# Optimization experiments

Hardware: AMD Instinct MI355X
Metric: run time of the kernel (lower is better)

The kernel has to match this reference:

```python
import jax, jax.numpy as jnp
import numpy as np

NUM_JOINTS = 33
EPS = 1e-5
# MediaPipe 33-landmark pose skeleton connections
SKELETON_EDGES = np.array([
    [0,1],[1,2],[2,3],[3,7],[0,4],[4,5],[5,6],[6,8],[9,10],
    [11,12],[11,13],[13,15],[15,17],[15,19],[15,21],[17,19],
    [12,14],[14,16],[16,18],[16,20],[16,22],[18,20],
    [11,23],[12,24],[23,24],[23,25],[24,26],[25,27],[26,28],
    [27,29],[28,30],[29,31],[30,32],[27,31],[28,32]], dtype=np.int64)


def _batched_edges(B):
    und = np.concatenate([SKELETON_EDGES, SKELETON_EDGES[:, ::-1]], axis=0)
    loops = np.stack([np.arange(NUM_JOINTS)] * 2, axis=1)
    e = np.concatenate([und, loops], axis=0)  # [103, 2] per graph (incl. self loops)
    eb = (e[None, :, :] + (np.arange(B) * NUM_JOINTS)[:, None, None]).reshape(-1, 2)
    return jnp.asarray(eb[:, 0], dtype=jnp.int32), jnp.asarray(eb[:, 1], dtype=jnp.int32)


def setup_inputs() -> dict:
    key = jax.random.key(0)
    B, N, F, H, L = 4096, NUM_JOINTS, 256, 256, 4
    ks = jax.random.split(key, 20)
    d = {"x": jax.random.normal(ks[0], (B, N, F), dtype=jnp.float32)}
    dims = [(F, H), (H, H), (H, H)]
    i = 1
    for li, (di, do) in enumerate(dims):
        d[f"w{li}"] = jax.random.normal(ks[i], (di, do), dtype=jnp.float32) * 0.05; i += 1
        d[f"b{li}"] = jnp.zeros((do,), dtype=jnp.float32)
        d[f"g{li}"] = jnp.ones((do,), dtype=jnp.float32)
        d[f"be{li}"] = jnp.zeros((do,), dtype=jnp.float32)
    d["wh"] = jax.random.normal(ks[i], (H, H), dtype=jnp.float32) * 0.05; i += 1
    d["bh"] = jnp.zeros((H,), dtype=jnp.float32)
    d["wc"] = jax.random.normal(ks[i], (H, L), dtype=jnp.float32) * 0.05; i += 1
    d["bc"] = jnp.zeros((L,), dtype=jnp.float32)
    src, dst = _batched_edges(B)
    d["src"], d["dst"] = src, dst
    return d


def _gcn_conv(x, W, b, src, dst, norm, num_nodes):
    h = x @ W                          # [NN, out]
    msg = h[src] * norm[:, None]       # gather + scale
    agg = jax.ops.segment_sum(msg, dst, num_segments=num_nodes)
    return agg + b


def _bn_relu(x, g, be):
    mu = jnp.mean(x, axis=0)
    var = jnp.mean((x - mu) ** 2, axis=0)  # biased, torch training BN
    return jax.nn.relu((x - mu) * jax.lax.rsqrt(var + EPS) * g + be)


def reference(x, w0, b0, g0, be0, w1, b1, g1, be1, w2, b2, g2, be2, wh, bh, wc, bc, src, dst):
    B, N, F = x.shape
    NN = B * N
    h = jnp.nan_to_num(x.reshape(NN, F))
    # symmetric GCN normalization D^{-1/2}(A+I)D^{-1/2}; self loops already in edge list
    deg = jax.ops.segment_sum(jnp.ones_like(src, dtype=h.dtype), dst, num_segments=NN)
    dinv = jax.lax.rsqrt(deg)
    norm = dinv[src] * dinv[dst]
    for W, b, g, be in ((w0, b0, g0, be0), (w1, b1, g1, be1), (w2, b2, g2, be2)):
        h = _gcn_conv(h, W, b, src, dst, norm, NN)
        h = _bn_relu(h, g, be)  # dropout: eval mode -> identity
    h = _gcn_conv(h, wh, bh, src, dst, norm, NN)
    pooled = h.reshape(B, N, -1).mean(axis=1)  # global mean pool per graph
    return pooled @ wc + bc
```

## Files before the change

### kernel.cpp

```cpp
#include <hip/hip_runtime.h>

typedef unsigned short u16;
typedef __attribute__((ext_vector_type(8))) short short8;
typedef __attribute__((ext_vector_type(4))) float floatx4;

#define NN_TOT 135168

static constexpr int NBCNT[33] = {2,2,2,2,2,2,2,1,1,1,1,3,3,2,2,4,4,2,2,2,2,1,1,3,3,2,2,3,3,2,2,2,2};
static constexpr int NBR[33][4] = {
 {1,4,0,0},{0,2,0,0},{1,3,0,0},{2,7,0,0},{0,5,0,0},{4,6,0,0},{5,8,0,0},
 {3,0,0,0},{6,0,0,0},{10,0,0,0},{9,0,0,0},
 {12,13,23,0},{11,14,24,0},{11,15,0,0},{12,16,0,0},
 {13,17,19,21},{14,18,20,22},
 {15,19,0,0},{16,20,0,0},{15,17,0,0},{16,18,0,0},{15,0,0,0},{16,0,0,0},
 {11,24,25,0},{12,23,26,0},{23,27,0,0},{24,28,0,0},
 {25,29,31,0},{26,30,32,0},{27,31,0,0},{28,32,0,0},{29,27,0,0},{30,28,0,0}};
static constexpr float R2 = 0.70710678f, R3 = 0.57735027f, R4 = 0.5f, R5 = 0.44721360f;
static constexpr float DINV[33] = {R3,R3,R3,R3,R3,R3,R3, R2,R2,R2,R2, R4,R4, R3,R3, R5,R5,
                                   R3,R3,R3,R3, R2,R2, R4,R4, R3,R3, R4,R4, R3,R3,R3,R3};

__device__ __forceinline__ float bf2f(u16 u) {
  unsigned int v = ((unsigned int)u) << 16; float f; __builtin_memcpy(&f, &v, 4); return f;
}
__device__ __forceinline__ u16 f2bf(float f) {
  unsigned int u; __builtin_memcpy(&u, &f, 4);
  return (u16)((u + 0x7fffu + ((u >> 16) & 1u)) >> 16);
}
__device__ __forceinline__ float ldin(const void* p, int i, int isbf) {
  return isbf ? bf2f(((const u16*)p)[i]) : ((const float*)p)[i];
}
__device__ __forceinline__ void gload_lds16(const u16* g, u16* l) {
  __builtin_amdgcn_global_load_lds((const __attribute__((address_space(1))) unsigned int*)g,
                                   (__attribute__((address_space(3))) unsigned int*)l, 16, 0, 0);
}

__global__ __launch_bounds__(256) void detect_kernel(const u16* __restrict__ x,
                                                     int* __restrict__ flag)
{
  __shared__ int cnt[256];
  const int t = threadIdx.x;
  int c = 0;
  for (int j = 0; j < 16; ++j) {
    u16 u = x[(t*16 + j)*2];
    int e = (u >> 7) & 0xFF;
    c += (e >= 118 && e <= 130) ? 1 : 0;
  }
  cnt[t] = c;
  __syncthreads();
  if (t == 0) {
    int s = 0;
    for (int i = 0; i < 256; ++i) s += cnt[i];
    *flag = (s > 2048) ? 1 : 0;
  }
}

__global__ __launch_bounds__(256) void transpose_kernel(const void* __restrict__ w0,
    const void* __restrict__ w1, const void* __restrict__ w2, u16* __restrict__ Wt,
    const int* __restrict__ flag)
{
  const int m = blockIdx.x >> 4;
  const int nb = (blockIdx.x & 15) * 16;
  const void* W = m == 0 ? w0 : (m == 1 ? w1 : w2);
  u16* O = Wt + (size_t)m * 65536;
  const int t = threadIdx.x;
  const int lane = t & 63, wv = t >> 6;
  const int isbf = *flag;
  if (isbf) {
    const u16* Wb = (const u16*)W;
#pragma unroll
    for (int nn = 0; nn < 4; ++nn) {
      const int n = nb + nn*4 + wv;
#pragma unroll
      for (int j = 0; j < 4; ++j) {
        const int k = lane + 64*j;
        O[n*256 + k] = Wb[k*256 + n];
      }
    }
  } else {
    const float* Wf = (const float*)W;
#pragma unroll
    for (int nn = 0; nn < 4; ++nn) {
      const int n = nb + nn*4 + wv;
#pragma unroll
      for (int j = 0; j < 4; ++j) {
        const int k = lane + 64*j;
        O[n*256 + k] = f2bf(Wf[k*256 + n]);
      }
    }
  }
}

__global__ __launch_bounds__(256) void init_kernel(const void* __restrict__ wh,
    const void* __restrict__ bh, const void* __restrict__ wc, const void* __restrict__ bc,
    float* __restrict__ wq, float* __restrict__ bq, float* __restrict__ repl,
    const int* __restrict__ flag)
{
  const int idx = blockIdx.x*256 + threadIdx.x;
  for (int i = idx; i < 3*64*512; i += 65*256) repl[i] = 0.f;
  const int isbf = *flag;
  const int t = threadIdx.x;
  const int lane = t & 63;
  if (blockIdx.x < 64) {
    const int r = blockIdx.x*4 + (t >> 6);
    float a0=0.f, a1=0.f, a2=0.f, a3=0.f;
#pragma unroll
    for (int j = 0; j < 4; ++j) {
      const int k = lane + 64*j;
      const float w = ldin(wh, r*256 + k, isbf);
      a0 += w*ldin(wc, k*4+0, isbf); a1 += w*ldin(wc, k*4+1, isbf);
      a2 += w*ldin(wc, k*4+2, isbf); a3 += w*ldin(wc, k*4+3, isbf);
    }
#pragma unroll
    for (int off = 32; off; off >>= 1) {
      a0 += __shfl_xor(a0, off); a1 += __shfl_xor(a1, off);
      a2 += __shfl_xor(a2, off); a3 += __shfl_xor(a3, off);
    }
    if (lane == 0) { wq[r*4+0]=a0; wq[r*4+1]=a1; wq[r*4+2]=a2; wq[r*4+3]=a3; }
  } else if (t < 64) {
    float s0=0.f, s1=0.f, s2=0.f, s3=0.f;
#pragma unroll
    for (int j = 0; j < 4; ++j) {
      const int k = lane + 64*j;
      const float b = ldin(bh, k, isbf);
      s0 += b*ldin(wc, k*4+0, isbf); s1 += b*ldin(wc, k*4+1, isbf);
      s2 += b*ldin(wc, k*4+2, isbf); s3 += b*ldin(wc, k*4+3, isbf);
    }
#pragma unroll
    for (int off = 32; off; off >>= 1) {
      s0 += __shfl_xor(s0, off); s1 += __shfl_xor(s1, off);
      s2 += __shfl_xor(s2, off); s3 += __shfl_xor(s3, off);
    }
    if (lane == 0) {
      bq[0] = s0 + ldin(bc, 0, isbf); bq[1] = s1 + ldin(bc, 1, isbf);
      bq[2] = s2 + ldin(bc, 2, isbf); bq[3] = s3 + ldin(bc, 3, isbf);
    }
  }
}

template<int ACT>
__global__ __launch_bounds__(256, 2) void gemm_kernel(
    const void* __restrict__ Ag, const u16* __restrict__ Bt,
    const float* __restrict__ fscale, const float* __restrict__ fshift,
    u16* __restrict__ T, const int* __restrict__ flag)
{
  __shared__ __align__(16) u16 sA[128*32];
  __shared__ __align__(16) u16 sB[256*32];
  const int tid = threadIdx.x;
  const int lane = tid & 63, wid = tid >> 6;
  const int wm = wid >> 1, wn = wid & 1;
  const size_t m0 = (size_t)blockIdx.x * 128;
  const int isbf = (ACT == 0) ? *flag : 1;

  floatx4 acc[4][8];
#pragma unroll
  for (int i = 0; i < 4; ++i)
#pragma unroll
    for (int j = 0; j < 8; ++j) acc[i][j] = (floatx4){0.f, 0.f, 0.f, 0.f};

  const int r0 = tid >> 2;
  const int c8 = (tid & 3) * 8;
  const int lr = lane >> 2;
  const int lc = (lane & 3) * 8;
  const int fr = lane & 15, q = lane >> 4;

  for (int kc = 0; kc < 8; ++kc) {
    const int k0 = kc * 32;
    __syncthreads();
    if (ACT == 0) {
      if (isbf) {
        const u16* Ab = (const u16*)Ag;
#pragma unroll
        for (int i = 0; i < 2; ++i)
          gload_lds16(Ab + (m0 + wid*32 + i*16 + lr)*256 + k0 + lc,
                      sA + (wid*32 + i*16)*32);
      } else {
        const float* Af = (const float*)Ag;
#pragma unroll
        for (int rr = 0; rr < 2; ++rr) {
          const int r = r0 + rr*64;
          float4 p0 = *(const float4*)(Af + (m0 + r)*256 + k0 + c8);
          float4 p1 = *(const float4*)(Af + (m0 + r)*256 + k0 + c8 + 4);
          u16 ov[8];
          ov[0]=f2bf(p0.x); ov[1]=f2bf(p0.y); ov[2]=f2bf(p0.z); ov[3]=f2bf(p0.w);
          ov[4]=f2bf(p1.x); ov[5]=f2bf(p1.y); ov[6]=f2bf(p1.z); ov[7]=f2bf(p1.w);
          *(uint4*)(sA + r*32 + c8) = *(const uint4*)ov;
        }
      }
    } else {
      const u16* Ab = (const u16*)Ag;
      float scv[8], shv[8];
#pragma unroll
      for (int j = 0; j < 8; ++j) { scv[j] = fscale[k0 + c8 + j]; shv[j] = fshift[k0 + c8 + j]; }
#pragma unroll
      for (int rr = 0; rr < 2; ++rr) {
        const int r = r0 + rr*64;
        uint4 pk = *(const uint4*)(Ab + (m0 + r)*256 + k0 + c8);
        const u16* us = (const u16*)&pk;
        u16 ov[8];
#pragma unroll
        for (int j = 0; j < 8; ++j) {
          float f = bf2f(us[j]);
          f = fmaxf(0.f, fmaf(f, scv[j], shv[j]));
          ov[j] = f2bf(f);
        }
        *(uint4*)(sA + r*32 + c8) = *(const uint4*)ov;
      }
    }
#pragma unroll
    for (int i = 0; i < 4; ++i)
      gload_lds16(Bt + (wid*64 + i*16 + lr)*256 + k0 + lc,
                  sB + (wid*64 + i*16)*32);
    __syncthreads();

    short8 a[4], b[8];
#pragma unroll
    for (int mf = 0; mf < 4; ++mf) a[mf] = *(const short8*)(sA + (wm*64 + mf*16 + fr)*32 + q*8);
#pragma unroll
    for (int nf = 0; nf < 8; ++nf) b[nf] = *(const short8*)(sB + (wn*128 + nf*16 + fr)*32 + q*8);
#pragma unroll
    for (int mf = 0; mf < 4; ++mf)
#pragma unroll
      for (int nf = 0; nf < 8; ++nf)
        acc[mf][nf] = __builtin_amdgcn_mfma_f32_16x16x32_bf16(a[mf], b[nf], acc[mf][nf], 0, 0, 0);
  }

#pragma unroll
  for (int mf = 0; mf < 4; ++mf)
#pragma unroll
    for (int nf = 0; nf < 8; ++nf)
#pragma unroll
      for (int r = 0; r < 4; ++r) {
        const size_t row = m0 + wm*64 + mf*16 + q*4 + r;
        const int col = wn*128 + nf*16 + fr;
        T[row*256 + col] = f2bf(acc[mf][nf][r]);
      }
}

__global__ __launch_bounds__(256) void agg_kernel(const u16* __restrict__ T,
    const void* __restrict__ bias, u16* __restrict__ H, float* __restrict__ repl,
    const int* __restrict__ flag)
{
  const int g = blockIdx.x, c = threadIdx.x;
  const int isbf = *flag;
  const u16* tg = T + (size_t)g * (33*256);
  u16* hg = H + (size_t)g * (33*256);
  float acc[33];
#pragma unroll
  for (int d = 0; d < 33; ++d) acc[d] = 0.f;
#pragma unroll
  for (int s = 0; s < 33; ++s) {
    float v = bf2f(tg[s*256 + c]) * DINV[s];
    acc[s] += v;
#pragma unroll
    for (int i = 0; i < NBCNT[s]; ++i) acc[NBR[s][i]] += v;
  }
  const float bv = ldin(bias, c, isbf);
  float s1 = 0.f, s2 = 0.f;
#pragma unroll
  for (int d = 0; d < 33; ++d) {
    float o = fmaf(acc[d], DINV[d], bv);
    hg[d*256 + c] = f2bf(o);
    s1 += o; s2 += o*o;
  }
  float* r1 = repl + (size_t)(g & 63) * 512;
  atomicAdd(r1 + c, s1);
  atomicAdd(r1 + 256 + c, s2);
}

__global__ __launch_bounds__(256) void statfin_kernel(const float* __restrict__ repl,
    const void* __restrict__ gamma, const void* __restrict__ beta, float* __restrict__ fs,
    const int* __restrict__ flag)
{
  const int c = threadIdx.x;
  const int isbf = *flag;
  float s1 = 0.f, s2 = 0.f;
  for (int r = 0; r < 64; ++r) { s1 += repl[r*512 + c]; s2 += repl[r*512 + 256 + c]; }
  const float inv = 1.f / (float)NN_TOT;
  const float mu = s1 * inv;
  const float var = s2 * inv - mu*mu;
  const float rs = rsqrtf(var + 1e-5f);
  const float sc = rs * ldin(gamma, c, isbf);
  fs[c] = sc;
  fs[256 + c] = ldin(beta, c, isbf) - mu * sc;
}

__global__ __launch_bounds__(256) void final_kernel(const u16* __restrict__ H,
    const float* __restrict__ fs, const float* __restrict__ wq,
    const float* __restrict__ bq, void* __restrict__ outp,
    const int* __restrict__ flag)
{
  const int g = blockIdx.x, c = threadIdx.x;
  const int isbf = *flag;
  const float sc = fs[c], sh = fs[256 + c];
  const u16* hg = H + (size_t)g * (33*256);
  float v = 0.f;
#pragma unroll
  for (int s = 0; s < 33; ++s) {
    float a = DINV[s];
#pragma unroll
    for (int i = 0; i < NBCNT[s]; ++i) a += DINV[NBR[s][i]];
    const float w = DINV[s] * a * (1.f/33.f);
    float x = bf2f(hg[s*256 + c]);
    x = fmaxf(0.f, fmaf(x, sc, sh));
    v += w * x;
  }
  float p0 = v*wq[c*4+0], p1 = v*wq[c*4+1], p2 = v*wq[c*4+2], p3 = v*wq[c*4+3];
#pragma unroll
  for (int off = 32; off; off >>= 1) {
    p0 += __shfl_xor(p0, off);
    p1 += __shfl_xor(p1, off);
    p2 += __shfl_xor(p2, off);
    p3 += __shfl_xor(p3, off);
  }
  __shared__ float sred[4][4];
  const int lane = c & 63, wid = c >> 6;
  if (lane == 0) { sred[wid][0]=p0; sred[wid][1]=p1; sred[wid][2]=p2; sred[wid][3]=p3; }
  __syncthreads();
  if (c < 4) {
    float r = sred[0][c] + sred[1][c] + sred[2][c] + sred[3][c] + bq[c];
    if (isbf) ((u16*)outp)[(size_t)g*4 + c] = f2bf(r);
    else      ((float*)outp)[(size_t)g*4 + c] = r;
  }
}

extern "C" void kernel_launch(void* const* d_in, const int* in_sizes, int n_in,
                              void* d_out, int out_size, void* d_ws, size_t ws_size,
                              hipStream_t stream)
{
  const void* x   = d_in[0];
  const void* w0  = d_in[1];
  const void* b0  = d_in[2];
  const void* g0  = d_in[3];
  const void* be0 = d_in[4];
  const void* w1  = d_in[5];
  const void* b1  = d_in[6];
  const void* g1  = d_in[7];
  const void* be1 = d_in[8];
  const void* w2  = d_in[9];
  const void* b2  = d_in[10];
  const void* g2  = d_in[11];
  const void* be2 = d_in[12];
  const void* wh  = d_in[13];
  const void* bh  = d_in[14];
  const void* wc  = d_in[15];
  const void* bc  = d_in[16];

  char* ws = (char*)d_ws;
  float* wq   = (float*)(ws + 0);
  float* bq   = (float*)(ws + 4096);
  float* fs   = (float*)(ws + 4608);
  int*   flag = (int*)  (ws + 12288);
  float* repl = (float*)(ws + 16384);
  u16*   Wt   = (u16*)  (ws + 409600);
  u16*   A    = (u16*)  (ws + 802816);
  (void)in_sizes; (void)n_in; (void)out_size; (void)ws_size;

  detect_kernel<<<1, 256, 0, stream>>>((const u16*)x, flag);
  transpose_kernel<<<48, 256, 0, stream>>>(w0, w1, w2, Wt, flag);
  init_kernel<<<65, 256, 0, stream>>>(wh, bh, wc, bc, wq, bq, repl, flag);

  gemm_kernel<0><<<1056, 256, 0, stream>>>(x, Wt, nullptr, nullptr, A, flag);
  agg_kernel<<<4096, 256, 0, stream>>>(A, b0, A, repl, flag);
  statfin_kernel<<<1, 256, 0, stream>>>(repl, g0, be0, fs, flag);
  gemm_kernel<1><<<1056, 256, 0, stream>>>(A, Wt + 65536, fs, fs + 256, A, flag);
  agg_kernel<<<4096, 256, 0, stream>>>(A, b1, A, repl + 32768, flag);
  statfin_kernel<<<1, 256, 0, stream>>>(repl + 32768, g1, be1, fs + 512, flag);
  gemm_kernel<1><<<1056, 256, 0, stream>>>(A, Wt + 131072, fs + 512, fs + 768, A, flag);
  agg_kernel<<<4096, 256, 0, stream>>>(A, b2, A, repl + 65536, flag);
  statfin_kernel<<<1, 256, 0, stream>>>(repl + 65536, g2, be2, fs + 1024, flag);
  final_kernel<<<4096, 256, 0, stream>>>(A, fs + 1024, wq, bq, d_out, flag);
}
```

Baseline: 454.2 us.

## Double-buffer GEMM LDS tiles and stage output through LDS for wide stores

Converts the GEMM main loop to a double-buffered scheme. The next K-chunk's global loads and the async LDS loads are issued before the MFMAs on the current buffer, and the BN/ReLU or fp32-to-bf16 conversion is written to the other buffer afterwards. This is meant to overlap memory latency with compute and cut one barrier per iteration. The epilogue now stages accumulator tiles through padded LDS so each thread writes 16-byte coalesced rows instead of scattered 2-byte stores. LDS use grows to 48KB per block, which may limit occupancy with launch_bounds(256,2). The scale and shift values are now reloaded per element inside finish rather than held in registers.

```diff
diff --git a/kernel.cpp b/kernel.cpp
--- a/kernel.cpp
+++ b/kernel.cpp
@@ -143,8 +143,9 @@
     const float* __restrict__ fscale, const float* __restrict__ fshift,
     u16* __restrict__ T, const int* __restrict__ flag)
 {
-  __shared__ __align__(16) u16 sA[128*32];
-  __shared__ __align__(16) u16 sB[256*32];
+  __shared__ __align__(16) u16 smem[24576];
+  u16* const sA0 = smem;
+  u16* const sB0 = smem + 8192;
   const int tid = threadIdx.x;
   const int lane = tid & 63, wid = tid >> 6;
   const int wm = wid >> 1, wn = wid & 1;
@@ -163,77 +164,108 @@
   const int lc = (lane & 3) * 8;
   const int fr = lane & 15, q = lane >> 4;
 
-  for (int kc = 0; kc < 8; ++kc) {
-    const int k0 = kc * 32;
-    __syncthreads();
-    if (ACT == 0) {
-      if (isbf) {
-        const u16* Ab = (const u16*)Ag;
-#pragma unroll
-        for (int i = 0; i < 2; ++i)
-          gload_lds16(Ab + (m0 + wid*32 + i*16 + lr)*256 + k0 + lc,
-                      sA + (wid*32 + i*16)*32);
-      } else {
-        const float* Af = (const float*)Ag;
-#pragma unroll
-        for (int rr = 0; rr < 2; ++rr) {
-          const int r = r0 + rr*64;
-          float4 p0 = *(const float4*)(Af + (m0 + r)*256 + k0 + c8);
-          float4 p1 = *(const float4*)(Af + (m0 + r)*256 + k0 + c8 + 4);
-          u16 ov[8];
-          ov[0]=f2bf(p0.x); ov[1]=f2bf(p0.y); ov[2]=f2bf(p0.z); ov[3]=f2bf(p0.w);
-          ov[4]=f2bf(p1.x); ov[5]=f2bf(p1.y); ov[6]=f2bf(p1.z); ov[7]=f2bf(p1.w);
-          *(uint4*)(sA + r*32 + c8) = *(const uint4*)ov;
-        }
+  const u16* Ab = (const u16*)Ag;
+  const float* Af = (const float*)Ag;
+
+  uint4  regA[2];
+  float4 regF[2][2];
+
+  auto issue = [&](int buf, int k0) {
+    if (ACT == 0 && isbf) {
+#pragma unroll
+      for (int i = 0; i < 2; ++i)
+        gload_lds16(Ab + (m0 + wid*32 + i*16 + lr)*256 + k0 + lc,
+                    sA0 + buf*4096 + (wid*32 + i*16)*32);
+    } else if (ACT == 0) {
+#pragma unroll
+      for (int rr = 0; rr < 2; ++rr) {
+        regF[rr][0] = *(const float4*)(Af + (m0 + r0 + rr*64)*256 + k0 + c8);
+        regF[rr][1] = *(const float4*)(Af + (m0 + r0 + rr*64)*256 + k0 + c8 + 4);
       }
     } else {
-      const u16* Ab = (const u16*)Ag;
-      float scv[8], shv[8];
-#pragma unroll
-      for (int j = 0; j < 8; ++j) { scv[j] = fscale[k0 + c8 + j]; shv[j] = fshift[k0 + c8 + j]; }
+#pragma unroll
+      for (int rr = 0; rr < 2; ++rr)
+        regA[rr] = *(const uint4*)(Ab + (m0 + r0 + rr*64)*256 + k0 + c8);
+    }
+#pragma unroll
+    for (int i = 0; i < 4; ++i)
+      gload_lds16(Bt + (wid*64 + i*16 + lr)*256 + k0 + lc,
+                  sB0 + buf*8192 + (wid*64 + i*16)*32);
+  };
+
+  auto finish = [&](int buf, int k0) {
+    if (ACT == 1) {
 #pragma unroll
       for (int rr = 0; rr < 2; ++rr) {
-        const int r = r0 + rr*64;
-        uint4 pk = *(const uint4*)(Ab + (m0 + r)*256 + k0 + c8);
-        const u16* us = (const u16*)&pk;
+        const u16* us = (const u16*)&regA[rr];
         u16 ov[8];
 #pragma unroll
         for (int j = 0; j < 8; ++j) {
           float f = bf2f(us[j]);
-          f = fmaxf(0.f, fmaf(f, scv[j], shv[j]));
+          f = fmaxf(0.f, fmaf(f, fscale[k0 + c8 + j], fshift[k0 + c8 + j]));
           ov[j] = f2bf(f);
         }
-        *(uint4*)(sA + r*32 + c8) = *(const uint4*)ov;
+        *(uint4*)(sA0 + buf*4096 + (r0 + rr*64)*32 + c8) = *(const uint4*)ov;
       }
-    }
-#pragma unroll
-    for (int i = 0; i < 4; ++i)
-      gload_lds16(Bt + (wid*64 + i*16 + lr)*256 + k0 + lc,
-                  sB + (wid*64 + i*16)*32);
-    __syncthreads();
+    } else if (ACT == 0 && !isbf) {
+#pragma unroll
+      for (int rr = 0; rr < 2; ++rr) {
+        u16 ov[8];
+        ov[0]=f2bf(regF[rr][0].x); ov[1]=f2bf(regF[rr][0].y);
+        ov[2]=f2bf(regF[rr][0].z); ov[3]=f2bf(regF[rr][0].w);
+        ov[4]=f2bf(regF[rr][1].x); ov[5]=f2bf(regF[rr][1].y);
+        ov[6]=f2bf(regF[rr][1].z); ov[7]=f2bf(regF[rr][1].w);
+        *(uint4*)(sA0 + buf*4096 + (r0 + rr*64)*32 + c8) = *(const uint4*)ov;
+      }
+    }
+  };
+
+  issue(0, 0);
+  finish(0, 0);
+  __syncthreads();
+
+  for (int kc = 0; kc < 8; ++kc) {
+    const int cur = kc & 1;
+    if (kc < 7) issue(cur ^ 1, (kc + 1) * 32);
 
     short8 a[4], b[8];
 #pragma unroll
-    for (int mf = 0; mf < 4; ++mf) a[mf] = *(const short8*)(sA + (wm*64 + mf*16 + fr)*32 + q*8);
-#pragma unroll
-    for (int nf = 0; nf < 8; ++nf) b[nf] = *(const short8*)(sB + (wn*128 + nf*16 + fr)*32 + q*8);
+    for (int mf = 0; mf < 4; ++mf)
+      a[mf] = *(const short8*)(sA0 + cur*4096 + (wm*64 + mf*16 + fr)*32 + q*8);
+#pragma unroll
+    for (int nf = 0; nf < 8; ++nf)
+      b[nf] = *(const short8*)(sB0 + cur*8192 + (wn*128 + nf*16 + fr)*32 + q*8);
 #pragma unroll
     for (int mf = 0; mf < 4; ++mf)
 #pragma unroll
       for (int nf = 0; nf < 8; ++nf)
         acc[mf][nf] = __builtin_amdgcn_mfma_f32_16x16x32_bf16(a[mf], b[nf], acc[mf][nf], 0, 0, 0);
-  }
-
-#pragma unroll
-  for (int mf = 0; mf < 4; ++mf)
+
+    if (kc < 7) { finish(cur ^ 1, (kc + 1) * 32); __syncthreads(); }
+  }
+
+  u16* const Ct = smem;
+  const int lrow = tid >> 3;
+  const int cg = (tid & 7) * 32;
+#pragma unroll
+  for (int mf = 0; mf < 4; ++mf) {
+    __syncthreads();
 #pragma unroll
     for (int nf = 0; nf < 8; ++nf)
 #pragma unroll
-      for (int r = 0; r < 4; ++r) {
-        const size_t row = m0 + wm*64 + mf*16 + q*4 + r;
-        const int col = wn*128 + nf*16 + fr;
-        T[row*256 + col] = f2bf(acc[mf][nf][r]);
-      }
+      for (int r = 0; r < 4; ++r)
+        Ct[(wm*16 + q*4 + r)*264 + wn*128 + nf*16 + fr] = f2bf(acc[mf][nf][r]);
+    __syncthreads();
+    const size_t grow = m0 + (size_t)((lrow >> 4) * 64 + mf*16 + (lrow & 15));
+    uint4 w0 = *(const uint4*)(Ct + lrow*264 + cg);
+    uint4 w1 = *(const uint4*)(Ct + lrow*264 + cg + 8);
+    uint4 w2 = *(const uint4*)(Ct + lrow*264 + cg + 16);
+    uint4 w3 = *(const uint4*)(Ct + lrow*264 + cg + 24);
+    *(uint4*)(T + grow*256 + cg)      = w0;
+    *(uint4*)(T + grow*256 + cg + 8)  = w1;
+    *(uint4*)(T + grow*256 + cg + 16) = w2;
+    *(uint4*)(T + grow*256 + cg + 24) = w3;
+  }
 }
 
 __global__ __launch_bounds__(256) void agg_kernel(const u16* __restrict__ T,
```

Result: slower. 479.2 us (+5.5%).

## Drop LDS staging in GEMM and load MFMA fragments directly from global

Applied to the files above, without the earlier changes.

The GEMM kernel no longer stages A and B tiles through shared memory. Each wave now owns 32 full rows across all 256 output columns, and it loads A and B fragments straight from global memory into registers, which removes both __syncthreads barriers. The aim is to cut LDS traffic and barrier stalls. The cost is that every wave re-reads the whole B matrix from global or cache through uncoalesced 16-byte loads, with less reuse between waves.

```diff
diff --git a/kernel.cpp b/kernel.cpp
--- a/kernel.cpp
+++ b/kernel.cpp
@@ -29,10 +29,6 @@
 __device__ __forceinline__ float ldin(const void* p, int i, int isbf) {
   return isbf ? bf2f(((const u16*)p)[i]) : ((const float*)p)[i];
 }
-__device__ __forceinline__ void gload_lds16(const u16* g, u16* l) {
-  __builtin_amdgcn_global_load_lds((const __attribute__((address_space(1))) unsigned int*)g,
-                                   (__attribute__((address_space(3))) unsigned int*)l, 16, 0, 0);
-}
 
 __global__ __launch_bounds__(256) void detect_kernel(const u16* __restrict__ x,
                                                      int* __restrict__ flag)
@@ -143,58 +139,53 @@
     const float* __restrict__ fscale, const float* __restrict__ fshift,
     u16* __restrict__ T, const int* __restrict__ flag)
 {
-  __shared__ __align__(16) u16 sA[128*32];
-  __shared__ __align__(16) u16 sB[256*32];
   const int tid = threadIdx.x;
-  const int lane = tid & 63, wid = tid >> 6;
-  const int wm = wid >> 1, wn = wid & 1;
+  const int lane = tid & 63, w = tid >> 6;
+  const int fr = lane & 15, q = lane >> 4;
   const size_t m0 = (size_t)blockIdx.x * 128;
+  const int rbase = w * 32;
   const int isbf = (ACT == 0) ? *flag : 1;
 
-  floatx4 acc[4][8];
-#pragma unroll
-  for (int i = 0; i < 4; ++i)
-#pragma unroll
-    for (int j = 0; j < 8; ++j) acc[i][j] = (floatx4){0.f, 0.f, 0.f, 0.f};
-
-  const int r0 = tid >> 2;
-  const int c8 = (tid & 3) * 8;
-  const int lr = lane >> 2;
-  const int lc = (lane & 3) * 8;
-  const int fr = lane & 15, q = lane >> 4;
+  const u16* Ab = (const u16*)Ag;
+  const float* Af = (const float*)Ag;
+
+  floatx4 acc[2][16];
+#pragma unroll
+  for (int i = 0; i < 2; ++i)
+#pragma unroll
+    for (int j = 0; j < 16; ++j) acc[i][j] = (floatx4){0.f, 0.f, 0.f, 0.f};
 
   for (int kc = 0; kc < 8; ++kc) {
     const int k0 = kc * 32;
-    __syncthreads();
+
+    short8 a[2];
     if (ACT == 0) {
       if (isbf) {
-        const u16* Ab = (const u16*)Ag;
-#pragma unroll
-        for (int i = 0; i < 2; ++i)
-          gload_lds16(Ab + (m0 + wid*32 + i*16 + lr)*256 + k0 + lc,
-                      sA + (wid*32 + i*16)*32);
+#pragma unroll
+        for (int mg = 0; mg < 2; ++mg)
+          a[mg] = *(const short8*)(Ab + (m0 + rbase + mg*16 + fr)*256 + k0 + q*8);
       } else {
-        const float* Af = (const float*)Ag;
-#pragma unroll
-        for (int rr = 0; rr < 2; ++rr) {
-          const int r = r0 + rr*64;
-          float4 p0 = *(const float4*)(Af + (m0 + r)*256 + k0 + c8);
-          float4 p1 = *(const float4*)(Af + (m0 + r)*256 + k0 + c8 + 4);
+#pragma unroll
+        for (int mg = 0; mg < 2; ++mg) {
+          const float* ap = Af + (m0 + rbase + mg*16 + fr)*256 + k0 + q*8;
+          float4 p0 = *(const float4*)(ap);
+          float4 p1 = *(const float4*)(ap + 4);
           u16 ov[8];
           ov[0]=f2bf(p0.x); ov[1]=f2bf(p0.y); ov[2]=f2bf(p0.z); ov[3]=f2bf(p0.w);
           ov[4]=f2bf(p1.x); ov[5]=f2bf(p1.y); ov[6]=f2bf(p1.z); ov[7]=f2bf(p1.w);
-          *(uint4*)(sA + r*32 + c8) = *(const uint4*)ov;
+          a[mg] = *(const short8*)ov;
         }
       }
     } else {
-      const u16* Ab = (const u16*)Ag;
-      float scv[8], shv[8];
-#pragma unroll
-      for (int j = 0; j < 8; ++j) { scv[j] = fscale[k0 + c8 + j]; shv[j] = fshift[k0 + c8 + j]; }
-#pragma unroll
-      for (int rr = 0; rr < 2; ++rr) {
-        const int r = r0 + rr*64;
-        uint4 pk = *(const uint4*)(Ab + (m0 + r)*256 + k0 + c8);
+      float4 sc0 = *(const float4*)(fscale + k0 + q*8);
+      float4 sc1 = *(const float4*)(fscale + k0 + q*8 + 4);
+      float4 sh0 = *(const float4*)(fshift + k0 + q*8);
+      float4 sh1 = *(const float4*)(fshift + k0 + q*8 + 4);
+      const float scv[8] = {sc0.x,sc0.y,sc0.z,sc0.w, sc1.x,sc1.y,sc1.z,sc1.w};
+      const float shv[8] = {sh0.x,sh0.y,sh0.z,sh0.w, sh1.x,sh1.y,sh1.z,sh1.w};
+#pragma unroll
+      for (int mg = 0; mg < 2; ++mg) {
+        uint4 pk = *(const uint4*)(Ab + (m0 + rbase + mg*16 + fr)*256 + k0 + q*8);
         const u16* us = (const u16*)&pk;
         u16 ov[8];
 #pragma unroll
@@ -203,36 +194,33 @@
           f = fmaxf(0.f, fmaf(f, scv[j], shv[j]));
           ov[j] = f2bf(f);
         }
-        *(uint4*)(sA + r*32 + c8) = *(const uint4*)ov;
-      }
-    }
-#pragma unroll
-    for (int i = 0; i < 4; ++i)
-      gload_lds16(Bt + (wid*64 + i*16 + lr)*256 + k0 + lc,
-                  sB + (wid*64 + i*16)*32);
-    __syncthreads();
-
-    short8 a[4], b[8];
-#pragma unroll
-    for (int mf = 0; mf < 4; ++mf) a[mf] = *(const short8*)(sA + (wm*64 + mf*16 + fr)*32 + q*8);
-#pragma unroll
-    for (int nf = 0; nf < 8; ++nf) b[nf] = *(const short8*)(sB + (wn*128 + nf*16 + fr)*32 + q*8);
-#pragma unroll
-    for (int mf = 0; mf < 4; ++mf)
+        a[mg] = *(const short8*)ov;
+      }
+    }
+
+#pragma unroll
+    for (int h = 0; h < 2; ++h) {
+      short8 b[8];
 #pragma unroll
       for (int nf = 0; nf < 8; ++nf)
-        acc[mf][nf] = __builtin_amdgcn_mfma_f32_16x16x32_bf16(a[mf], b[nf], acc[mf][nf], 0, 0, 0);
-  }
-
-#pragma unroll
-  for (int mf = 0; mf < 4; ++mf)
-#pragma unroll
-    for (int nf = 0; nf < 8; ++nf)
+        b[nf] = *(const short8*)(Bt + (h*128 + nf*16 + fr)*256 + k0 + q*8);
+#pragma unroll
+      for (int mg = 0; mg < 2; ++mg)
+#pragma unroll
+        for (int nf = 0; nf < 8; ++nf)
+          acc[mg][h*8 + nf] =
+            __builtin_amdgcn_mfma_f32_16x16x32_bf16(a[mg], b[nf], acc[mg][h*8 + nf], 0, 0, 0);
+    }
+  }
+
+#pragma unroll
+  for (int mg = 0; mg < 2; ++mg)
+#pragma unroll
+    for (int n = 0; n < 16; ++n)
 #pragma unroll
       for (int r = 0; r < 4; ++r) {
-        const size_t row = m0 + wm*64 + mf*16 + q*4 + r;
-        const int col = wn*128 + nf*16 + fr;
-        T[row*256 + col] = f2bf(acc[mf][nf][r]);
+        const size_t row = m0 + rbase + mg*16 + q*4 + r;
+        T[row*256 + n*16 + fr] = f2bf(acc[mg][n][r]);
       }
 }
 
```

New measurement: 596.5 us. 1.31x slower.

## Fuse GCN GEMM with graph aggregation and BN statistics per two-graph block

Applied to the files above, without the earlier changes.

Each block now computes the feature transform for two whole 33-node graphs (66 rows) with MFMA. It stages the result tile in LDS and then runs the skeleton aggregation, bias add and BN partial-sum atomics directly from shared memory. This removes the separate aggregation kernel and the global write and re-read of the intermediate bf16 matrix for each layer. In exchange, the MFMA tiles pad 33 rows to 48, which wastes some matrix compute. Each thread also keeps two 33-entry accumulator arrays, which raises register pressure.

```diff
diff --git a/kernel.cpp b/kernel.cpp
--- a/kernel.cpp
+++ b/kernel.cpp
@@ -138,63 +138,87 @@
 }
 
 template<int ACT>
-__global__ __launch_bounds__(256, 2) void gemm_kernel(
+__global__ __launch_bounds__(256, 2) void fused_kernel(
     const void* __restrict__ Ag, const u16* __restrict__ Bt,
     const float* __restrict__ fscale, const float* __restrict__ fshift,
-    u16* __restrict__ T, const int* __restrict__ flag)
-{
-  __shared__ __align__(16) u16 sA[128*32];
-  __shared__ __align__(16) u16 sB[256*32];
+    const void* __restrict__ bias, u16* __restrict__ H,
+    float* __restrict__ repl, const int* __restrict__ flag)
+{
+  __shared__ __align__(16) u16 smem[17424];
+  u16* const sA = smem;
+  u16* const sB = smem + 3072;
   const int tid = threadIdx.x;
-  const int lane = tid & 63, wid = tid >> 6;
-  const int wm = wid >> 1, wn = wid & 1;
-  const size_t m0 = (size_t)blockIdx.x * 128;
-  const int isbf = (ACT == 0) ? *flag : 1;
-
-  floatx4 acc[4][8];
-#pragma unroll
-  for (int i = 0; i < 4; ++i)
-#pragma unroll
-    for (int j = 0; j < 8; ++j) acc[i][j] = (floatx4){0.f, 0.f, 0.f, 0.f};
+  const int lane = tid & 63, w = tid >> 6;
+  const int gi = w >> 1, h = w & 1;
+  const int fr = lane & 15, q = lane >> 4;
+  const size_t R0 = (size_t)blockIdx.x * 66;
+  const int dtf = *flag;
+  const int isbf = (ACT == 0) ? dtf : 1;
+
+  const u16* Ab = (const u16*)Ag;
+  const float* Af = (const float*)Ag;
+
+  floatx4 acc[3][8];
+#pragma unroll
+  for (int t = 0; t < 3; ++t)
+#pragma unroll
+    for (int j = 0; j < 8; ++j) acc[t][j] = (floatx4){0.f, 0.f, 0.f, 0.f};
 
   const int r0 = tid >> 2;
   const int c8 = (tid & 3) * 8;
   const int lr = lane >> 2;
   const int lc = (lane & 3) * 8;
-  const int fr = lane & 15, q = lane >> 4;
 
   for (int kc = 0; kc < 8; ++kc) {
     const int k0 = kc * 32;
     __syncthreads();
-    if (ACT == 0) {
-      if (isbf) {
-        const u16* Ab = (const u16*)Ag;
-#pragma unroll
-        for (int i = 0; i < 2; ++i)
-          gload_lds16(Ab + (m0 + wid*32 + i*16 + lr)*256 + k0 + lc,
-                      sA + (wid*32 + i*16)*32);
-      } else {
-        const float* Af = (const float*)Ag;
-#pragma unroll
-        for (int rr = 0; rr < 2; ++rr) {
-          const int r = r0 + rr*64;
-          float4 p0 = *(const float4*)(Af + (m0 + r)*256 + k0 + c8);
-          float4 p1 = *(const float4*)(Af + (m0 + r)*256 + k0 + c8 + 4);
-          u16 ov[8];
-          ov[0]=f2bf(p0.x); ov[1]=f2bf(p0.y); ov[2]=f2bf(p0.z); ov[3]=f2bf(p0.w);
-          ov[4]=f2bf(p1.x); ov[5]=f2bf(p1.y); ov[6]=f2bf(p1.z); ov[7]=f2bf(p1.w);
-          *(uint4*)(sA + r*32 + c8) = *(const uint4*)ov;
+    if (ACT == 0 && isbf) {
+      gload_lds16(Ab + (R0 + w*16 + lr)*256 + k0 + lc, sA + (w*16)*32);
+      if (w == 0) {
+        size_t rg = R0 + 64 + lr;
+        if (rg >= NN_TOT) rg = NN_TOT - 1;
+        if (lane < 8)
+          gload_lds16(Ab + rg*256 + k0 + lc, sA + 64*32);
+      }
+    } else if (ACT == 0) {
+      {
+        const float* ap = Af + (R0 + r0)*256 + k0 + c8;
+        float4 p0 = *(const float4*)(ap);
+        float4 p1 = *(const float4*)(ap + 4);
+        u16 ov[8];
+        ov[0]=f2bf(p0.x); ov[1]=f2bf(p0.y); ov[2]=f2bf(p0.z); ov[3]=f2bf(p0.w);
+        ov[4]=f2bf(p1.x); ov[5]=f2bf(p1.y); ov[6]=f2bf(p1.z); ov[7]=f2bf(p1.w);
+        *(uint4*)(sA + r0*32 + c8) = *(const uint4*)ov;
+      }
+      if (tid < 8) {
+        const int r = 64 + (tid >> 2);
+        const float* ap = Af + (R0 + r)*256 + k0 + c8;
+        float4 p0 = *(const float4*)(ap);
+        float4 p1 = *(const float4*)(ap + 4);
+        u16 ov[8];
+        ov[0]=f2bf(p0.x); ov[1]=f2bf(p0.y); ov[2]=f2bf(p0.z); ov[3]=f2bf(p0.w);
+        ov[4]=f2bf(p1.x); ov[5]=f2bf(p1.y); ov[6]=f2bf(p1.z); ov[7]=f2bf(p1.w);
+        *(uint4*)(sA + r*32 + c8) = *(const uint4*)ov;
+      }
+    } else {
+      float scv[8], shv[8];
+#pragma unroll
+      for (int j = 0; j < 8; ++j) { scv[j] = fscale[k0 + c8 + j]; shv[j] = fshift[k0 + c8 + j]; }
+      {
+        uint4 pk = *(const uint4*)(Ab + (R0 + r0)*256 + k0 + c8);
+        const u16* us = (const u16*)&pk;
+        u16 ov[8];
+#pragma unroll
+        for (int j = 0; j < 8; ++j) {
+          float f = bf2f(us[j]);
+          f = fmaxf(0.f, fmaf(f, scv[j], shv[j]));
+          ov[j] = f2bf(f);
         }
-      }
-    } else {
-      const u16* Ab = (const u16*)Ag;
-      float scv[8], shv[8];
-#pragma unroll
-      for (int j = 0; j < 8; ++j) { scv[j] = fscale[k0 + c8 + j]; shv[j] = fshift[k0 + c8 + j]; }
-#pragma unroll
-      for (int rr = 0; rr < 2; ++rr) {
-        const int r = r0 + rr*64;
-        uint4 pk = *(const uint4*)(Ab + (m0 + r)*256 + k0 + c8);
+        *(uint4*)(sA + r0*32 + c8) = *(const uint4*)ov;
+      }
+      if (tid < 8) {
+        const int r = 64 + (tid >> 2);
+        uint4 pk = *(const uint4*)(Ab + (R0 + r)*256 + k0 + c8);
         const u16* us = (const u16*)&pk;
         u16 ov[8];
 #pragma unroll
@@ -208,63 +232,69 @@
     }
 #pragma unroll
     for (int i = 0; i < 4; ++i)
-      gload_lds16(Bt + (wid*64 + i*16 + lr)*256 + k0 + lc,
-                  sB + (wid*64 + i*16)*32);
+      gload_lds16(Bt + (w*64 + i*16 + lr)*256 + k0 + lc,
+                  sB + (w*64 + i*16)*32);
     __syncthreads();
 
-    short8 a[4], b[8];
-#pragma unroll
-    for (int mf = 0; mf < 4; ++mf) a[mf] = *(const short8*)(sA + (wm*64 + mf*16 + fr)*32 + q*8);
-#pragma unroll
-    for (int nf = 0; nf < 8; ++nf) b[nf] = *(const short8*)(sB + (wn*128 + nf*16 + fr)*32 + q*8);
-#pragma unroll
-    for (int mf = 0; mf < 4; ++mf)
+    short8 a[3], b[8];
+#pragma unroll
+    for (int t = 0; t < 3; ++t)
+      a[t] = *(const short8*)(sA + (gi*33 + t*16 + fr)*32 + q*8);
+#pragma unroll
+    for (int nf = 0; nf < 8; ++nf)
+      b[nf] = *(const short8*)(sB + (h*128 + nf*16 + fr)*32 + q*8);
+#pragma unroll
+    for (int t = 0; t < 3; ++t)
 #pragma unroll
       for (int nf = 0; nf < 8; ++nf)
-        acc[mf][nf] = __builtin_amdgcn_mfma_f32_16x16x32_bf16(a[mf], b[nf], acc[mf][nf], 0, 0, 0);
-  }
-
-#pragma unroll
-  for (int mf = 0; mf < 4; ++mf)
+        acc[t][nf] = __builtin_amdgcn_mfma_f32_16x16x32_bf16(a[t], b[nf], acc[t][nf], 0, 0, 0);
+  }
+
+  __syncthreads();
+  u16* const Tl = smem;
+#pragma unroll
+  for (int t = 0; t < 3; ++t)
 #pragma unroll
     for (int nf = 0; nf < 8; ++nf)
 #pragma unroll
       for (int r = 0; r < 4; ++r) {
-        const size_t row = m0 + wm*64 + mf*16 + q*4 + r;
-        const int col = wn*128 + nf*16 + fr;
-        T[row*256 + col] = f2bf(acc[mf][nf][r]);
-      }
-}
-
-__global__ __launch_bounds__(256) void agg_kernel(const u16* __restrict__ T,
-    const void* __restrict__ bias, u16* __restrict__ H, float* __restrict__ repl,
-    const int* __restrict__ flag)
-{
-  const int g = blockIdx.x, c = threadIdx.x;
-  const int isbf = *flag;
-  const u16* tg = T + (size_t)g * (33*256);
-  u16* hg = H + (size_t)g * (33*256);
-  float acc[33];
-#pragma unroll
-  for (int d = 0; d < 33; ++d) acc[d] = 0.f;
+        const int row = t*16 + q*4 + r;
+        if (row < 33)
+          Tl[(gi*33 + row)*264 + h*128 + nf*16 + fr] = f2bf(acc[t][nf][r]);
+      }
+  __syncthreads();
+
+  const int g2 = tid >> 7, cp = tid & 127;
+  const size_t Gg = (size_t)blockIdx.x*2 + g2;
+  float a0[33], a1[33];
+#pragma unroll
+  for (int d = 0; d < 33; ++d) { a0[d] = 0.f; a1[d] = 0.f; }
 #pragma unroll
   for (int s = 0; s < 33; ++s) {
-    float v = bf2f(tg[s*256 + c]) * DINV[s];
-    acc[s] += v;
-#pragma unroll
-    for (int i = 0; i < NBCNT[s]; ++i) acc[NBR[s][i]] += v;
-  }
-  const float bv = ldin(bias, c, isbf);
-  float s1 = 0.f, s2 = 0.f;
+    const unsigned int pk = *(const unsigned int*)(Tl + (g2*33 + s)*264 + cp*2);
+    const float v0 = bf2f((u16)(pk & 0xffffu)) * DINV[s];
+    const float v1 = bf2f((u16)(pk >> 16)) * DINV[s];
+    a0[s] += v0; a1[s] += v1;
+#pragma unroll
+    for (int i = 0; i < NBCNT[s]; ++i) { a0[NBR[s][i]] += v0; a1[NBR[s][i]] += v1; }
+  }
+  const float bv0 = ldin(bias, cp*2,     dtf);
+  const float bv1 = ldin(bias, cp*2 + 1, dtf);
+  float s10 = 0.f, s20 = 0.f, s11 = 0.f, s21 = 0.f;
+  u16* hg = H + Gg * (33*256);
 #pragma unroll
   for (int d = 0; d < 33; ++d) {
-    float o = fmaf(acc[d], DINV[d], bv);
-    hg[d*256 + c] = f2bf(o);
-    s1 += o; s2 += o*o;
-  }
-  float* r1 = repl + (size_t)(g & 63) * 512;
-  atomicAdd(r1 + c, s1);
-  atomicAdd(r1 + 256 + c, s2);
+    const float o0 = fmaf(a0[d], DINV[d], bv0);
+    const float o1 = fmaf(a1[d], DINV[d], bv1);
+    const unsigned int pw = (unsigned int)f2bf(o0) | ((unsigned int)f2bf(o1) << 16);
+    *(unsigned int*)(hg + d*256 + cp*2) = pw;
+    s10 += o0; s20 += o0*o0; s11 += o1; s21 += o1*o1;
+  }
+  float* r1p = repl + (Gg & 63)*512;
+  atomicAdd(r1p + cp*2,           s10);
+  atomicAdd(r1p + cp*2 + 1,       s11);
+  atomicAdd(r1p + 256 + cp*2,     s20);
+  atomicAdd(r1p + 256 + cp*2 + 1, s21);
 }
 
 __global__ __launch_bounds__(256) void statfin_kernel(const float* __restrict__ repl,
@@ -359,14 +389,11 @@
   transpose_kernel<<<48, 256, 0, stream>>>(w0, w1, w2, Wt, flag);
   init_kernel<<<65, 256, 0, stream>>>(wh, bh, wc, bc, wq, bq, repl, flag);
 
-  gemm_kernel<0><<<1056, 256, 0, stream>>>(x, Wt, nullptr, nullptr, A, flag);
-  agg_kernel<<<4096, 256, 0, stream>>>(A, b0, A, repl, flag);
+  fused_kernel<0><<<2048, 256, 0, stream>>>(x, Wt, nullptr, nullptr, b0, A, repl, flag);
   statfin_kernel<<<1, 256, 0, stream>>>(repl, g0, be0, fs, flag);
-  gemm_kernel<1><<<1056, 256, 0, stream>>>(A, Wt + 65536, fs, fs + 256, A, flag);
-  agg_kernel<<<4096, 256, 0, stream>>>(A, b1, A, repl + 32768, flag);
+  fused_kernel<1><<<2048, 256, 0, stream>>>(A, Wt + 65536, fs, fs + 256, b1, A, repl + 32768, flag);
   statfin_kernel<<<1, 256, 0, stream>>>(repl + 32768, g1, be1, fs + 512, flag);
-  gemm_kernel<1><<<1056, 256, 0, stream>>>(A, Wt + 131072, fs + 512, fs + 768, A, flag);
-  agg_kernel<<<4096, 256, 0, stream>>>(A, b2, A, repl + 65536, flag);
+  fused_kernel<1><<<2048, 256, 0, stream>>>(A, Wt + 131072, fs + 512, fs + 768, b2, A, repl + 65536, flag);
   statfin_kernel<<<1, 256, 0, stream>>>(repl + 65536, g2, be2, fs + 1024, flag);
   final_kernel<<<4096, 256, 0, stream>>>(A, fs + 1024, wq, bq, d_out, flag);
 }
```

Measured after the change: 448.3 us. Within noise of the previous version (-1.3%).
